# Kernel tuning notes

Hardware: AMD Instinct MI355X
Metric: run time of the kernel (lower is better)

The kernel has to match this reference:

```python
import jax, jax.numpy as jnp
import numpy as np

B, T, N_EMBED, HEAD = 512, 256, 384, 64
BLOCK = 256
SCALE = N_EMBED ** -0.5  # source scales by input-channel dim, not head_size


def setup_inputs() -> dict:
    key = jax.random.key(0)
    kx, kk, kq, kv = jax.random.split(key, 4)
    x = jax.random.normal(kx, (B, T, N_EMBED), dtype=jnp.float32)
    # torch Linear(n_embed, head_size, bias=False) weights, stored as (in, out)
    s = N_EMBED ** -0.5
    Wk = jax.random.normal(kk, (N_EMBED, HEAD), dtype=jnp.float32) * s
    Wq = jax.random.normal(kq, (N_EMBED, HEAD), dtype=jnp.float32) * s
    Wv = jax.random.normal(kv, (N_EMBED, HEAD), dtype=jnp.float32) * s
    return {"x": x, "Wk": Wk, "Wq": Wq, "Wv": Wv}


def reference(x, Wk, Wq, Wv):
    Bx, Tx, _ = x.shape
    K = jnp.einsum('btc,ch->bth', x, Wk)
    Q = jnp.einsum('btc,ch->bth', x, Wq)
    V = jnp.einsum('btc,ch->bth', x, Wv)
    scores = jnp.einsum('bth,bsh->bts', Q, K) * SCALE  # [B, T, T]
    causal = jnp.tril(jnp.ones((Tx, Tx), dtype=bool))
    scores = jnp.where(causal[None, :, :], scores, -jnp.inf)
    W = jax.nn.softmax(scores, axis=-1)
    # dropout is identity in eval mode (reference baseline is deterministic)
    out = jnp.einsum('bts,bsh->bth', W, V)
    return out
```

## Files before the change

kernel.cpp:

```cpp
#include <hip/hip_runtime.h>
#include <hip/hip_bf16.h>

#define B_  512
#define T_  256
#define C_  384
#define H_  64
#define SCALE_ 0.05103103630798287f

typedef float f32x4  __attribute__((ext_vector_type(4)));
typedef short bf16x8 __attribute__((ext_vector_type(8)));
typedef short bf16x4 __attribute__((ext_vector_type(4)));

__device__ __forceinline__ unsigned short f2bf(float f) {
    union { float f; unsigned u; } v; v.f = f;
    unsigned r = v.u + 0x7FFFu + ((v.u >> 16) & 1u);
    return (unsigned short)(r >> 16);
}

__device__ __forceinline__ int swz64(int row, int col) {
    return row * 64 + (((col >> 3) ^ (row & 7)) << 3) + (col & 7);
}

__global__ __launch_bounds__(1024, 4) void att_head_kernel(
    const float* __restrict__ x,  const float* __restrict__ Wk,
    const float* __restrict__ Wq, const float* __restrict__ Wv,
    float* __restrict__ out)
{
    __shared__ __align__(16) short smem[67584];
    short* const wst0 = smem;
    short* const wst1 = smem + 12288;
    short* const Qs   = smem;
    short* const Pb   = smem + 24576;
    short* const Ks   = smem + 34816;
    short* const Vt   = smem + 51200;

    const int tid  = threadIdx.x;
    const int b    = blockIdx.x;
    const int w    = tid >> 6;
    const int lane = tid & 63;
    const int g    = lane >> 4;
    const int i    = lane & 15;
    const int rb   = 16 * w;

    const float* xb = x + (size_t)b * T_ * C_;
    const float* Wm[3] = { Wk, Wq, Wv };

    f32x4 accP[12];
    #pragma unroll
    for (int nb = 0; nb < 12; nb++) accP[nb] = f32x4{0.f, 0.f, 0.f, 0.f};

    const float* xrow = xb + (size_t)(rb + i) * C_ + g * 8;

    auto stageW = [&](int kc, short* buf) {
        #pragma unroll
        for (int m = 0; m < 3; m++) {
            const float* Wp = Wm[m] + (size_t)(kc + w * 4) * H_ + lane;
            bf16x4 pk;
            #pragma unroll
            for (int jj = 0; jj < 4; jj++) pk[jj] = (short)f2bf(Wp[jj * H_]);
            const int row = m * 64 + lane;
            const int k0  = w * 4;
            *(bf16x4*)&buf[row * 64 + (((k0 >> 3) ^ (row & 7)) << 3) + (k0 & 7)] = pk;
        }
    };

    float4 xr[2][4];
    #pragma unroll
    for (int ks = 0; ks < 2; ks++)
        #pragma unroll
        for (int h = 0; h < 2; h++)
            xr[0][ks * 2 + h] = *(const float4*)(xrow + ks * 32 + h * 4);
    stageW(0, wst0);
    asm volatile("s_waitcnt lgkmcnt(0)\n\ts_barrier" ::: "memory");

    #pragma unroll
    for (int j = 0; j < 6; j++) {
        const int par = j & 1;
        short* cur = par ? wst1 : wst0;
        if (j < 5) {
            #pragma unroll
            for (int ks = 0; ks < 2; ks++)
                #pragma unroll
                for (int h = 0; h < 2; h++)
                    xr[par ^ 1][ks * 2 + h] = *(const float4*)(xrow + (j + 1) * 64 + ks * 32 + h * 4);
            stageW((j + 1) * 64, par ? wst0 : wst1);
        }
        bf16x8 afs[2];
        #pragma unroll
        for (int ks = 0; ks < 2; ks++)
            #pragma unroll
            for (int h = 0; h < 2; h++) {
                const float4 v = xr[par][ks * 2 + h];
                afs[ks][h * 4 + 0] = (short)f2bf(v.x);
                afs[ks][h * 4 + 1] = (short)f2bf(v.y);
                afs[ks][h * 4 + 2] = (short)f2bf(v.z);
                afs[ks][h * 4 + 3] = (short)f2bf(v.w);
            }
        #pragma unroll
        for (int nb = 0; nb < 12; nb++)
            #pragma unroll
            for (int ks = 0; ks < 2; ks++) {
                const int brow = nb * 16 + i;
                const bf16x8 bfr = *(const bf16x8*)&cur[brow * 64 + (((ks * 4 + g) ^ (i & 7)) << 3)];
                accP[nb] = __builtin_amdgcn_mfma_f32_16x16x32_bf16(afs[ks], bfr, accP[nb], 0, 0, 0);
            }
        asm volatile("s_waitcnt lgkmcnt(0)\n\ts_barrier" ::: "memory");
    }

    #pragma unroll
    for (int nb = 0; nb < 4; nb++)
        #pragma unroll
        for (int r = 0; r < 4; r++)
            Ks[swz64(rb + 4 * g + r, nb * 16 + i)] = (short)f2bf(accP[nb][r]);
    #pragma unroll
    for (int nb = 0; nb < 4; nb++)
        #pragma unroll
        for (int r = 0; r < 4; r++)
            Qs[swz64(rb + 4 * g + r, nb * 16 + i)] = (short)f2bf(accP[4 + nb][r]);
    #pragma unroll
    for (int nb = 0; nb < 4; nb++) {
        const int hrow = nb * 16 + i;
        const int t0   = rb + 4 * g;
        bf16x4 pk;
        #pragma unroll
        for (int r = 0; r < 4; r++) pk[r] = (short)f2bf(accP[8 + nb][r]);
        const int blk = t0 >> 3;
        *(bf16x4*)&Vt[hrow * 256 + (((blk & ~7) | ((blk ^ (hrow & 7)) & 7)) << 3) + (t0 & 7)] = pk;
    }
    asm volatile("s_waitcnt lgkmcnt(0)\n\ts_barrier" ::: "memory");

    bf16x8 qf[2];
    #pragma unroll
    for (int ks = 0; ks < 2; ks++)
        qf[ks] = *(const bf16x8*)&Qs[(rb + i) * 64 + (((ks * 4 + g) ^ (i & 7)) << 3)];

    short* myP = Pb + w * 640;
    const float NEG_INF = -__builtin_inff();
    const int lim = w;

    f32x4 accS[16];
    #pragma unroll
    for (int nt = 0; nt < 16; nt++) accS[nt] = f32x4{0.f, 0.f, 0.f, 0.f};

    #pragma unroll
    for (int nt = 0; nt < 16; nt++) {
        if (nt <= lim) {
            #pragma unroll
            for (int ks = 0; ks < 2; ks++) {
                const bf16x8 kf = *(const bf16x8*)&Ks[(nt * 16 + i) * 64 + (((ks * 4 + g) ^ (i & 7)) << 3)];
                accS[nt] = __builtin_amdgcn_mfma_f32_16x16x32_bf16(qf[ks], kf, accS[nt], 0, 0, 0);
            }
        }
    }

    float mrow[4] = { NEG_INF, NEG_INF, NEG_INF, NEG_INF };
    #pragma unroll
    for (int nt = 0; nt < 16; nt++)
        #pragma unroll
        for (int r = 0; r < 4; r++) {
            const int col = nt * 16 + i;
            const int row = rb + 4 * g + r;
            float v = accS[nt][r] * SCALE_;
            v = (col <= row) ? v : NEG_INF;
            accS[nt][r] = v;
            mrow[r] = fmaxf(mrow[r], v);
        }
    #pragma unroll
    for (int r = 0; r < 4; r++)
        #pragma unroll
        for (int msk = 1; msk < 16; msk <<= 1)
            mrow[r] = fmaxf(mrow[r], __shfl_xor(mrow[r], msk, 64));

    float lsum[4] = { 0.f, 0.f, 0.f, 0.f };
    #pragma unroll
    for (int nt = 0; nt < 16; nt++)
        #pragma unroll
        for (int r = 0; r < 4; r++) {
            const float p = __expf(accS[nt][r] - mrow[r]);
            accS[nt][r] = p;
            lsum[r] += p;
        }
    #pragma unroll
    for (int r = 0; r < 4; r++)
        #pragma unroll
        for (int msk = 1; msk < 16; msk <<= 1)
            lsum[r] += __shfl_xor(lsum[r], msk, 64);

    f32x4 accO[4];
    #pragma unroll
    for (int ht = 0; ht < 4; ht++) accO[ht] = f32x4{0.f, 0.f, 0.f, 0.f};

    #pragma unroll
    for (int ck = 0; ck < 8; ck++) {
        if (2 * ck <= lim) {
            #pragma unroll
            for (int t2 = 0; t2 < 2; t2++)
                #pragma unroll
                for (int r = 0; r < 4; r++) {
                    const int q = 4 * g + r, kk = t2 * 16 + i;
                    myP[q * 40 + ((((kk >> 3) ^ (q >> 2)) & 3) << 3) + (kk & 7)] =
                        (short)f2bf(accS[2 * ck + t2][r]);
                }
            asm volatile("s_waitcnt lgkmcnt(0)" ::: "memory");
            const bf16x8 pf = *(const bf16x8*)&myP[i * 40 + (((g ^ (i >> 2)) & 3) << 3)];
            #pragma unroll
            for (int ht = 0; ht < 4; ht++) {
                const int hrow = ht * 16 + i;
                const int blk  = ck * 4 + g;
                const bf16x8 vf = *(const bf16x8*)&Vt[hrow * 256 +
                        (((blk & ~7) | ((blk ^ (hrow & 7)) & 7)) << 3)];
                accO[ht] = __builtin_amdgcn_mfma_f32_16x16x32_bf16(pf, vf, accO[ht], 0, 0, 0);
            }
        }
    }

    float inv[4];
    #pragma unroll
    for (int r = 0; r < 4; r++) inv[r] = 1.f / lsum[r];
    #pragma unroll
    for (int ht = 0; ht < 4; ht++)
        #pragma unroll
        for (int r = 0; r < 4; r++) {
            const int row = rb + 4 * g + r;
            out[((size_t)b * T_ + row) * H_ + ht * 16 + i] = accO[ht][r] * inv[r];
        }
}

extern "C" void kernel_launch(void* const* d_in, const int* in_sizes, int n_in,
                              void* d_out, int out_size, void* d_ws, size_t ws_size,
                              hipStream_t stream) {
    const float* x  = (const float*)d_in[0];
    const float* Wk = (const float*)d_in[1];
    const float* Wq = (const float*)d_in[2];
    const float* Wv = (const float*)d_in[3];
    float* out = (float*)d_out;
    (void)d_ws; (void)ws_size; (void)in_sizes; (void)n_in; (void)out_size;
    att_head_kernel<<<dim3(B_), dim3(1024), 0, stream>>>(x, Wk, Wq, Wv, out);
}
```

Before: 60.22 us.

## Retile QKV projection to 32x96 warp tiles with packed bf16 conversion

The projection GEMM now gives each wave a 32-row by 96-column output tile instead of 16 rows by all 192 columns. Each W fragment read from LDS then feeds two MFMAs, which halves LDS reads per MFMA for the B operand. Conversions of x and W use the hardware v_cvt_pk_bf16_f32 instruction instead of software rounding. Global loads for the next chunk are issued before the MFMAs, and their conversion and LDS write are deferred until after them so load latency overlaps compute. The cost is more x loads per wave (two row blocks) and more registers held for the raw fp32 values.

Result: slower. 76.60 us (+27.2%).

```diff
diff --git a/kernel.cpp b/kernel.cpp
--- a/kernel.cpp
+++ b/kernel.cpp
@@ -15,6 +15,12 @@
     union { float f; unsigned u; } v; v.f = f;
     unsigned r = v.u + 0x7FFFu + ((v.u >> 16) & 1u);
     return (unsigned short)(r >> 16);
+}
+
+__device__ __forceinline__ unsigned cvt_pk_bf16(float lo, float hi) {
+    unsigned r;
+    asm("v_cvt_pk_bf16_f32 %0, %1, %2" : "=v"(r) : "v"(lo), "v"(hi));
+    return r;
 }
 
 __device__ __forceinline__ int swz64(int row, int col) {
@@ -40,95 +46,122 @@
     const int lane = tid & 63;
     const int g    = lane >> 4;
     const int i    = lane & 15;
-    const int rb   = 16 * w;
+    const int wr   = w >> 1;
+    const int wc   = w & 1;
 
     const float* xb = x + (size_t)b * T_ * C_;
     const float* Wm[3] = { Wk, Wq, Wv };
 
-    f32x4 accP[12];
-    #pragma unroll
-    for (int nb = 0; nb < 12; nb++) accP[nb] = f32x4{0.f, 0.f, 0.f, 0.f};
-
-    const float* xrow = xb + (size_t)(rb + i) * C_ + g * 8;
-
-    auto stageW = [&](int kc, short* buf) {
+    f32x4 accP[2][6];
+    #pragma unroll
+    for (int m = 0; m < 2; m++)
+        #pragma unroll
+        for (int nb = 0; nb < 6; nb++) accP[m][nb] = f32x4{0.f, 0.f, 0.f, 0.f};
+
+    const float* xrow0 = xb + (size_t)(32 * wr + i) * C_ + g * 8;
+    const float* xrow1 = xrow0 + 16 * C_;
+
+    float4 xrf[2][2][2];
+    float  wf[3][4];
+
+    auto loadX = [&](int kc) {
+        #pragma unroll
+        for (int ks = 0; ks < 2; ks++)
+            #pragma unroll
+            for (int h = 0; h < 2; h++) {
+                xrf[0][ks][h] = *(const float4*)(xrow0 + kc + ks * 32 + h * 4);
+                xrf[1][ks][h] = *(const float4*)(xrow1 + kc + ks * 32 + h * 4);
+            }
+    };
+    auto loadW = [&](int kc) {
         #pragma unroll
         for (int m = 0; m < 3; m++) {
             const float* Wp = Wm[m] + (size_t)(kc + w * 4) * H_ + lane;
-            bf16x4 pk;
-            #pragma unroll
-            for (int jj = 0; jj < 4; jj++) pk[jj] = (short)f2bf(Wp[jj * H_]);
+            #pragma unroll
+            for (int jj = 0; jj < 4; jj++) wf[m][jj] = Wp[jj * H_];
+        }
+    };
+    auto writeW = [&](short* buf) {
+        #pragma unroll
+        for (int m = 0; m < 3; m++) {
             const int row = m * 64 + lane;
             const int k0  = w * 4;
+            bf16x4 pk;
+            union { unsigned u; short s[2]; } p0, p1;
+            p0.u = cvt_pk_bf16(wf[m][0], wf[m][1]);
+            p1.u = cvt_pk_bf16(wf[m][2], wf[m][3]);
+            pk[0] = p0.s[0]; pk[1] = p0.s[1]; pk[2] = p1.s[0]; pk[3] = p1.s[1];
             *(bf16x4*)&buf[row * 64 + (((k0 >> 3) ^ (row & 7)) << 3) + (k0 & 7)] = pk;
         }
     };
 
-    float4 xr[2][4];
-    #pragma unroll
-    for (int ks = 0; ks < 2; ks++)
-        #pragma unroll
-        for (int h = 0; h < 2; h++)
-            xr[0][ks * 2 + h] = *(const float4*)(xrow + ks * 32 + h * 4);
-    stageW(0, wst0);
+    loadX(0); loadW(0);
+    writeW(wst0);
     asm volatile("s_waitcnt lgkmcnt(0)\n\ts_barrier" ::: "memory");
 
     #pragma unroll
     for (int j = 0; j < 6; j++) {
-        const int par = j & 1;
-        short* cur = par ? wst1 : wst0;
-        if (j < 5) {
-            #pragma unroll
-            for (int ks = 0; ks < 2; ks++)
-                #pragma unroll
-                for (int h = 0; h < 2; h++)
-                    xr[par ^ 1][ks * 2 + h] = *(const float4*)(xrow + (j + 1) * 64 + ks * 32 + h * 4);
-            stageW((j + 1) * 64, par ? wst0 : wst1);
-        }
-        bf16x8 afs[2];
-        #pragma unroll
-        for (int ks = 0; ks < 2; ks++)
-            #pragma unroll
-            for (int h = 0; h < 2; h++) {
-                const float4 v = xr[par][ks * 2 + h];
-                afs[ks][h * 4 + 0] = (short)f2bf(v.x);
-                afs[ks][h * 4 + 1] = (short)f2bf(v.y);
-                afs[ks][h * 4 + 2] = (short)f2bf(v.z);
-                afs[ks][h * 4 + 3] = (short)f2bf(v.w);
-            }
-        #pragma unroll
-        for (int nb = 0; nb < 12; nb++)
+        short* const cur = (j & 1) ? wst1 : wst0;
+        short* const alt = (j & 1) ? wst0 : wst1;
+
+        bf16x8 afs[2][2];
+        #pragma unroll
+        for (int m = 0; m < 2; m++)
             #pragma unroll
             for (int ks = 0; ks < 2; ks++) {
-                const int brow = nb * 16 + i;
+                union { bf16x8 v; unsigned u[4]; } a;
+                a.u[0] = cvt_pk_bf16(xrf[m][ks][0].x, xrf[m][ks][0].y);
+                a.u[1] = cvt_pk_bf16(xrf[m][ks][0].z, xrf[m][ks][0].w);
+                a.u[2] = cvt_pk_bf16(xrf[m][ks][1].x, xrf[m][ks][1].y);
+                a.u[3] = cvt_pk_bf16(xrf[m][ks][1].z, xrf[m][ks][1].w);
+                afs[m][ks] = a.v;
+            }
+
+        if (j < 5) { loadX((j + 1) * 64); loadW((j + 1) * 64); }
+
+        #pragma unroll
+        for (int nb = 0; nb < 6; nb++) {
+            const int brow = 96 * wc + 16 * nb + i;
+            #pragma unroll
+            for (int ks = 0; ks < 2; ks++) {
                 const bf16x8 bfr = *(const bf16x8*)&cur[brow * 64 + (((ks * 4 + g) ^ (i & 7)) << 3)];
-                accP[nb] = __builtin_amdgcn_mfma_f32_16x16x32_bf16(afs[ks], bfr, accP[nb], 0, 0, 0);
-            }
+                accP[0][nb] = __builtin_amdgcn_mfma_f32_16x16x32_bf16(afs[0][ks], bfr, accP[0][nb], 0, 0, 0);
+                accP[1][nb] = __builtin_amdgcn_mfma_f32_16x16x32_bf16(afs[1][ks], bfr, accP[1][nb], 0, 0, 0);
+            }
+        }
+
+        if (j < 5) writeW(alt);
         asm volatile("s_waitcnt lgkmcnt(0)\n\ts_barrier" ::: "memory");
     }
 
     #pragma unroll
-    for (int nb = 0; nb < 4; nb++)
-        #pragma unroll
-        for (int r = 0; r < 4; r++)
-            Ks[swz64(rb + 4 * g + r, nb * 16 + i)] = (short)f2bf(accP[nb][r]);
-    #pragma unroll
-    for (int nb = 0; nb < 4; nb++)
-        #pragma unroll
-        for (int r = 0; r < 4; r++)
-            Qs[swz64(rb + 4 * g + r, nb * 16 + i)] = (short)f2bf(accP[4 + nb][r]);
-    #pragma unroll
-    for (int nb = 0; nb < 4; nb++) {
-        const int hrow = nb * 16 + i;
-        const int t0   = rb + 4 * g;
-        bf16x4 pk;
-        #pragma unroll
-        for (int r = 0; r < 4; r++) pk[r] = (short)f2bf(accP[8 + nb][r]);
-        const int blk = t0 >> 3;
-        *(bf16x4*)&Vt[hrow * 256 + (((blk & ~7) | ((blk ^ (hrow & 7)) & 7)) << 3) + (t0 & 7)] = pk;
+    for (int m = 0; m < 2; m++) {
+        const int row0 = 32 * wr + 16 * m + 4 * g;
+        #pragma unroll
+        for (int nb = 0; nb < 6; nb++) {
+            const int gc = 96 * wc + 16 * nb;
+            if (gc < 64) {
+                #pragma unroll
+                for (int r = 0; r < 4; r++)
+                    Ks[swz64(row0 + r, gc + i)] = (short)f2bf(accP[m][nb][r]);
+            } else if (gc < 128) {
+                #pragma unroll
+                for (int r = 0; r < 4; r++)
+                    Qs[swz64(row0 + r, gc - 64 + i)] = (short)f2bf(accP[m][nb][r]);
+            } else {
+                const int hrow = gc - 128 + i;
+                const int t0   = row0;
+                bf16x4 pk;
+                #pragma unroll
+                for (int r = 0; r < 4; r++) pk[r] = (short)f2bf(accP[m][nb][r]);
+                const int blk = t0 >> 3;
+                *(bf16x4*)&Vt[hrow * 256 + (((blk & ~7) | ((blk ^ (hrow & 7)) & 7)) << 3) + (t0 & 7)] = pk;
+            }
+        }
     }
     asm volatile("s_waitcnt lgkmcnt(0)\n\ts_barrier" ::: "memory");
 
+    const int rb = 16 * w;
     bf16x8 qf[2];
     #pragma unroll
     for (int ks = 0; ks < 2; ks++)
```

## Restructure attention into transposed online-softmax pipeline with double-buffered P tiles

Applied to the files above, without the earlier changes.

Reworks the attention phase to compute S transposed (K·Q) so each lane owns one query row. It processes key tiles in pairs using an online softmax with a lazy rescale threshold, and software-pipelines the P·V MFMA of the previous pair with the score computation of the current one. Q is read from shared memory into registers before K overwrites the same buffer, which shrinks LDS use. V is stored with a padded layout instead of a swizzle, P is converted with packed bf16 instructions, and the output is written with float4 stores. In exchange, register and control complexity rise, and a deferred rescale could lose precision if scores grow inside the threshold.

New measurement: 57.49 us. 4.5% less time.

```diff
diff --git a/kernel.cpp b/kernel.cpp
--- a/kernel.cpp
+++ b/kernel.cpp
@@ -17,6 +17,12 @@
     return (unsigned short)(r >> 16);
 }
 
+__device__ __forceinline__ unsigned cvt_pk_bf16(float lo, float hi) {
+    unsigned r;
+    asm("v_cvt_pk_bf16_f32 %0, %1, %2" : "=v"(r) : "v"(lo), "v"(hi));
+    return r;
+}
+
 __device__ __forceinline__ int swz64(int row, int col) {
     return row * 64 + (((col >> 3) ^ (row & 7)) << 3) + (col & 7);
 }
@@ -26,13 +32,12 @@
     const float* __restrict__ Wq, const float* __restrict__ Wv,
     float* __restrict__ out)
 {
-    __shared__ __align__(16) short smem[67584];
+    __shared__ __align__(16) short smem[53760];
     short* const wst0 = smem;
     short* const wst1 = smem + 12288;
-    short* const Qs   = smem;
-    short* const Pb   = smem + 24576;
-    short* const Ks   = smem + 34816;
-    short* const Vt   = smem + 51200;
+    short* const Ks   = smem;
+    short* const Vt   = smem + 16384;
+    short* const Pb   = smem + 33280;
 
     const int tid  = threadIdx.x;
     const int b    = blockIdx.x;
@@ -97,13 +102,14 @@
                 afs[ks][h * 4 + 3] = (short)f2bf(v.w);
             }
         #pragma unroll
-        for (int nb = 0; nb < 12; nb++)
+        for (int nb = 0; nb < 12; nb++) {
             #pragma unroll
             for (int ks = 0; ks < 2; ks++) {
                 const int brow = nb * 16 + i;
                 const bf16x8 bfr = *(const bf16x8*)&cur[brow * 64 + (((ks * 4 + g) ^ (i & 7)) << 3)];
                 accP[nb] = __builtin_amdgcn_mfma_f32_16x16x32_bf16(afs[ks], bfr, accP[nb], 0, 0, 0);
             }
+        }
         asm volatile("s_waitcnt lgkmcnt(0)\n\ts_barrier" ::: "memory");
     }
 
@@ -111,119 +117,117 @@
     for (int nb = 0; nb < 4; nb++)
         #pragma unroll
         for (int r = 0; r < 4; r++)
-            Ks[swz64(rb + 4 * g + r, nb * 16 + i)] = (short)f2bf(accP[nb][r]);
+            Ks[swz64(rb + 4 * g + r, 16 * nb + i)] = (short)f2bf(accP[4 + nb][r]);
+    asm volatile("s_waitcnt lgkmcnt(0)" ::: "memory");
+    bf16x8 qf[2];
+    #pragma unroll
+    for (int ks = 0; ks < 2; ks++)
+        qf[ks] = *(const bf16x8*)&Ks[(rb + i) * 64 + (((4 * ks + g) ^ (i & 7)) << 3)];
+    asm volatile("s_waitcnt lgkmcnt(0)" ::: "memory");
     #pragma unroll
     for (int nb = 0; nb < 4; nb++)
         #pragma unroll
         for (int r = 0; r < 4; r++)
-            Qs[swz64(rb + 4 * g + r, nb * 16 + i)] = (short)f2bf(accP[4 + nb][r]);
+            Ks[swz64(rb + 4 * g + r, 16 * nb + i)] = (short)f2bf(accP[nb][r]);
     #pragma unroll
     for (int nb = 0; nb < 4; nb++) {
-        const int hrow = nb * 16 + i;
-        const int t0   = rb + 4 * g;
         bf16x4 pk;
         #pragma unroll
         for (int r = 0; r < 4; r++) pk[r] = (short)f2bf(accP[8 + nb][r]);
-        const int blk = t0 >> 3;
-        *(bf16x4*)&Vt[hrow * 256 + (((blk & ~7) | ((blk ^ (hrow & 7)) & 7)) << 3) + (t0 & 7)] = pk;
+        *(bf16x4*)&Vt[(16 * nb + i) * 264 + rb + 4 * g] = pk;
     }
     asm volatile("s_waitcnt lgkmcnt(0)\n\ts_barrier" ::: "memory");
 
-    bf16x8 qf[2];
-    #pragma unroll
-    for (int ks = 0; ks < 2; ks++)
-        qf[ks] = *(const bf16x8*)&Qs[(rb + i) * 64 + (((ks * 4 + g) ^ (i & 7)) << 3)];
-
-    short* myP = Pb + w * 640;
+    short* const myP = Pb + w * 1280;
     const float NEG_INF = -__builtin_inff();
-    const int lim = w;
-
-    f32x4 accS[16];
-    #pragma unroll
-    for (int nt = 0; nt < 16; nt++) accS[nt] = f32x4{0.f, 0.f, 0.f, 0.f};
-
-    #pragma unroll
-    for (int nt = 0; nt < 16; nt++) {
-        if (nt <= lim) {
-            #pragma unroll
-            for (int ks = 0; ks < 2; ks++) {
-                const bf16x8 kf = *(const bf16x8*)&Ks[(nt * 16 + i) * 64 + (((ks * 4 + g) ^ (i & 7)) << 3)];
-                accS[nt] = __builtin_amdgcn_mfma_f32_16x16x32_bf16(qf[ks], kf, accS[nt], 0, 0, 0);
-            }
-        }
-    }
-
-    float mrow[4] = { NEG_INF, NEG_INF, NEG_INF, NEG_INF };
-    #pragma unroll
-    for (int nt = 0; nt < 16; nt++)
-        #pragma unroll
-        for (int r = 0; r < 4; r++) {
-            const int col = nt * 16 + i;
-            const int row = rb + 4 * g + r;
-            float v = accS[nt][r] * SCALE_;
-            v = (col <= row) ? v : NEG_INF;
-            accS[nt][r] = v;
-            mrow[r] = fmaxf(mrow[r], v);
-        }
-    #pragma unroll
-    for (int r = 0; r < 4; r++)
-        #pragma unroll
-        for (int msk = 1; msk < 16; msk <<= 1)
-            mrow[r] = fmaxf(mrow[r], __shfl_xor(mrow[r], msk, 64));
-
-    float lsum[4] = { 0.f, 0.f, 0.f, 0.f };
-    #pragma unroll
-    for (int nt = 0; nt < 16; nt++)
-        #pragma unroll
-        for (int r = 0; r < 4; r++) {
-            const float p = __expf(accS[nt][r] - mrow[r]);
-            accS[nt][r] = p;
-            lsum[r] += p;
-        }
-    #pragma unroll
-    for (int r = 0; r < 4; r++)
-        #pragma unroll
-        for (int msk = 1; msk < 16; msk <<= 1)
-            lsum[r] += __shfl_xor(lsum[r], msk, 64);
-
+    float mrun = NEG_INF, lrun = 0.f;
     f32x4 accO[4];
     #pragma unroll
     for (int ht = 0; ht < 4; ht++) accO[ht] = f32x4{0.f, 0.f, 0.f, 0.f};
 
-    #pragma unroll
-    for (int ck = 0; ck < 8; ck++) {
-        if (2 * ck <= lim) {
-            #pragma unroll
-            for (int t2 = 0; t2 < 2; t2++)
+    auto PVADD = [&](int bufsel, int ck) {
+        const bf16x8 pf = *(const bf16x8*)&myP[bufsel * 640 + i * 40 + 8 * g];
+        #pragma unroll
+        for (int ht = 0; ht < 4; ht++) {
+            const bf16x8 vf = *(const bf16x8*)&Vt[(16 * ht + i) * 264 + 32 * ck + 8 * g];
+            accO[ht] = __builtin_amdgcn_mfma_f32_16x16x32_bf16(vf, pf, accO[ht], 0, 0, 0);
+        }
+    };
+
+    const int npair = w >> 1;
+    #pragma unroll
+    for (int p = 0; p < 8; p++) {
+        if (p <= npair) {
+            f32x4 sA[2];
+            sA[0] = f32x4{0.f, 0.f, 0.f, 0.f};
+            sA[1] = f32x4{0.f, 0.f, 0.f, 0.f};
+            #pragma unroll
+            for (int s = 0; s < 2; s++) {
+                const int nt = 2 * p + s;
+                if (nt <= w) {
+                    #pragma unroll
+                    for (int ks = 0; ks < 2; ks++) {
+                        const bf16x8 kfr = *(const bf16x8*)&Ks[(16 * nt + i) * 64 +
+                                (((4 * ks + g) ^ (i & 7)) << 3)];
+                        sA[s] = __builtin_amdgcn_mfma_f32_16x16x32_bf16(kfr, qf[ks], sA[s], 0, 0, 0);
+                    }
+                }
+            }
+            if (p > 0) PVADD((p - 1) & 1, p - 1);
+
+            float mt = NEG_INF;
+            #pragma unroll
+            for (int s = 0; s < 2; s++)
                 #pragma unroll
                 for (int r = 0; r < 4; r++) {
-                    const int q = 4 * g + r, kk = t2 * 16 + i;
-                    myP[q * 40 + ((((kk >> 3) ^ (q >> 2)) & 3) << 3) + (kk & 7)] =
-                        (short)f2bf(accS[2 * ck + t2][r]);
+                    const int kv = 16 * (2 * p + s) + 4 * g + r;
+                    const bool ok = (2 * p + s <= w) && (kv <= rb + i);
+                    const float v = ok ? sA[s][r] * SCALE_ : NEG_INF;
+                    sA[s][r] = v;
+                    mt = fmaxf(mt, v);
                 }
-            asm volatile("s_waitcnt lgkmcnt(0)" ::: "memory");
-            const bf16x8 pf = *(const bf16x8*)&myP[i * 40 + (((g ^ (i >> 2)) & 3) << 3)];
-            #pragma unroll
-            for (int ht = 0; ht < 4; ht++) {
-                const int hrow = ht * 16 + i;
-                const int blk  = ck * 4 + g;
-                const bf16x8 vf = *(const bf16x8*)&Vt[hrow * 256 +
-                        (((blk & ~7) | ((blk ^ (hrow & 7)) & 7)) << 3)];
-                accO[ht] = __builtin_amdgcn_mfma_f32_16x16x32_bf16(pf, vf, accO[ht], 0, 0, 0);
-            }
-        }
-    }
-
-    float inv[4];
-    #pragma unroll
-    for (int r = 0; r < 4; r++) inv[r] = 1.f / lsum[r];
-    #pragma unroll
-    for (int ht = 0; ht < 4; ht++)
-        #pragma unroll
-        for (int r = 0; r < 4; r++) {
-            const int row = rb + 4 * g + r;
-            out[((size_t)b * T_ + row) * H_ + ht * 16 + i] = accO[ht][r] * inv[r];
-        }
+            mt = fmaxf(mt, __shfl_xor(mt, 16, 64));
+            mt = fmaxf(mt, __shfl_xor(mt, 32, 64));
+
+            if (!__all(mt <= mrun + 8.0f)) {
+                const float mnew = fmaxf(mrun, mt);
+                const float f = __expf(mrun - mnew);
+                mrun = mnew; lrun *= f;
+                #pragma unroll
+                for (int ht = 0; ht < 4; ht++)
+                    #pragma unroll
+                    for (int r = 0; r < 4; r++) accO[ht][r] *= f;
+            }
+            #pragma unroll
+            for (int s = 0; s < 2; s++) {
+                const float p0 = __expf(sA[s][0] - mrun);
+                const float p1 = __expf(sA[s][1] - mrun);
+                const float p2 = __expf(sA[s][2] - mrun);
+                const float p3 = __expf(sA[s][3] - mrun);
+                lrun += (p0 + p1) + (p2 + p3);
+                union { bf16x4 v; unsigned u[2]; } pk;
+                pk.u[0] = cvt_pk_bf16(p0, p1);
+                pk.u[1] = cvt_pk_bf16(p2, p3);
+                *(bf16x4*)&myP[(p & 1) * 640 + i * 40 + 16 * s + 4 * g] = pk.v;
+            }
+        }
+    }
+    PVADD(npair & 1, npair);
+
+    lrun += __shfl_xor(lrun, 16, 64);
+    lrun += __shfl_xor(lrun, 32, 64);
+    const float inv = 1.f / lrun;
+
+    float* orow = out + ((size_t)b * T_ + rb + i) * H_;
+    #pragma unroll
+    for (int ht = 0; ht < 4; ht++) {
+        float4 o;
+        o.x = accO[ht][0] * inv;
+        o.y = accO[ht][1] * inv;
+        o.z = accO[ht][2] * inv;
+        o.w = accO[ht][3] * inv;
+        *(float4*)&orow[16 * ht + 4 * g] = o;
+    }
 }
 
 extern "C" void kernel_launch(void* const* d_in, const int* in_sizes, int n_in,
```
